# Performance work log

Hardware: AMD Instinct MI355X
Metric: run time of the kernel (lower is better)

The kernel has to match this reference:

```python
import jax, jax.numpy as jnp
import numpy as np

BETA = 0.25
N_EMBED = 8192
DIM = 256


def setup_inputs() -> dict:
    key = jax.random.key(0)
    k1, k2 = jax.random.split(key)
    z = jax.random.normal(k1, (16, DIM, 32, 32), dtype=jnp.float32)
    # nn.Embedding init: uniform(-1/n_embed, 1/n_embed)
    codebook = jax.random.uniform(
        k2, (N_EMBED, DIM), dtype=jnp.float32,
        minval=-1.0 / N_EMBED, maxval=1.0 / N_EMBED)
    return {"z": z, "codebook": codebook}


def reference(z, codebook):
    # b c h w -> b h w c
    zp = jnp.transpose(z, (0, 2, 3, 1))
    b, h, w, c = zp.shape
    zf = zp.reshape(-1, c)  # [N, dim]
    # squared L2 distances: ||z||^2 + ||e||^2 - 2 z.e
    d = (jnp.sum(zf * zf, axis=1, keepdims=True)
         + jnp.sum(codebook * codebook, axis=1)
         - 2.0 * jnp.einsum('nd,kd->nk', zf, codebook))  # [N, n_embed]
    idx = jnp.argmin(d, axis=1)  # [N]
    z_q = codebook[idx].reshape(b, h, w, c)
    loss = (BETA * jnp.mean((jax.lax.stop_gradient(z_q) - zp) ** 2)
            + jnp.mean((z_q - jax.lax.stop_gradient(zp)) ** 2))
    # straight-through estimator
    z_q = zp + jax.lax.stop_gradient(z_q - zp)
    z_q = jnp.transpose(z_q, (0, 3, 1, 2))  # b h w c -> b c h w
    return z_q, loss, idx
```

## Files before the change

kernel.cpp:

```cpp
#include <hip/hip_runtime.h>
#include <cfloat>


#define NROWS 16384
#define NCODE 8192
#define DIMC  256
#define HW    1024
#define ZQN   4194304

#define ZT_OFF   0
#define CBT_OFF  2097152
#define ZSQ_OFF  3145728
#define CAND_OFF 3162112
#define LOSS_OFF ZQN
#define IDX_OFF  (ZQN + 1)

#define NSLICE 8
#define PRUNE_T 4300u
#define ZSCALE 2097152.0f

typedef __attribute__((ext_vector_type(8))) short bf16x8;
typedef __attribute__((ext_vector_type(4))) float f32x4;
typedef __attribute__((ext_vector_type(4))) unsigned int uint4v;

__device__ __forceinline__ unsigned umax(unsigned a, unsigned b) { return a > b ? a : b; }
__device__ __forceinline__ unsigned umin(unsigned a, unsigned b) { return a < b ? a : b; }

__device__ __forceinline__ unsigned short f2bf(float f) {
    unsigned u = __float_as_uint(f);
    return (unsigned short)((u + 0x7fffu + ((u >> 16) & 1u)) >> 16);
}

#define GLD_LDS16(gptr, lptr) \
  __builtin_amdgcn_global_load_lds((const __attribute__((address_space(1))) unsigned int*)(const void*)(gptr), \
                                   (__attribute__((address_space(3))) unsigned int*)(lptr), 16, 0, 0)

__global__ void prep_kernel(const float* __restrict__ z, const float* __restrict__ cb,
                            float* __restrict__ out) {
    int bid = blockIdx.x;
    int tid = threadIdx.x;
    if (bid < 1024) {
        __shared__ unsigned short lds[64 * 65];
        unsigned short* zt = (unsigned short*)(out + ZT_OFF);
        int c0 = (bid & 3) * 64;
        int n0 = (bid >> 2) * 64;
        const float* zb = z + (size_t)(n0 >> 10) * (DIMC * HW) + (n0 & 1023);
        #pragma unroll
        for (int i = 0; i < 4; ++i) {
            int f = tid + i * 256;
            int cl = f >> 4, n4 = f & 15;
            float4 v = *(const float4*)(zb + (size_t)(c0 + cl) * HW + n4 * 4);
            lds[(n4 * 4 + 0) * 65 + cl] = f2bf(v.x * ZSCALE);
            lds[(n4 * 4 + 1) * 65 + cl] = f2bf(v.y * ZSCALE);
            lds[(n4 * 4 + 2) * 65 + cl] = f2bf(v.z * ZSCALE);
            lds[(n4 * 4 + 3) * 65 + cl] = f2bf(v.w * ZSCALE);
        }
        __syncthreads();
        #pragma unroll
        for (int i = 0; i < 2; ++i) {
            int f = tid + i * 256;
            int nl = f >> 3, oct = f & 7;
            const unsigned short* p = lds + nl * 65 + oct * 8;
            uint4v u;
            u.x = (unsigned)p[0] | ((unsigned)p[1] << 16);
            u.y = (unsigned)p[2] | ((unsigned)p[3] << 16);
            u.z = (unsigned)p[4] | ((unsigned)p[5] << 16);
            u.w = (unsigned)p[6] | ((unsigned)p[7] << 16);
            *(uint4v*)(zt + (size_t)(n0 + nl) * DIMC + c0 + oct * 8) = u;
        }
    } else if (bid < 2048) {
        unsigned short* cbt = (unsigned short*)(out + CBT_OFF);
        size_t t = (size_t)(bid - 1024) * 256 + tid;
        float4 a = *(const float4*)(cb + t * 8);
        float4 b = *(const float4*)(cb + t * 8 + 4);
        uint4v u;
        u.x = (unsigned)f2bf(a.x) | ((unsigned)f2bf(a.y) << 16);
        u.y = (unsigned)f2bf(a.z) | ((unsigned)f2bf(a.w) << 16);
        u.z = (unsigned)f2bf(b.x) | ((unsigned)f2bf(b.y) << 16);
        u.w = (unsigned)f2bf(b.z) | ((unsigned)f2bf(b.w) << 16);
        *(uint4v*)(cbt + t * 8) = u;
        if (bid == 1024 && tid == 0) out[LOSS_OFF] = 0.0f;
    } else {
        int n = (bid - 2048) * 256 + tid;
        const float* zp = z + (size_t)(n >> 10) * (DIMC * HW) + (n & 1023);
        double s = 0.0;
        for (int c = 0; c < DIMC; ++c) {
            double v = (double)zp[(size_t)c * HW];
            s += v * v;
        }
        out[ZSQ_OFF + n] = (float)s;
    }
}

__global__ __launch_bounds__(256, 2)
void argmin_kernel(float* __restrict__ out) {
    __shared__ __align__(16) unsigned short a_s[2 * 32 * 256];
    const unsigned short* zt  = (const unsigned short*)(out + ZT_OFF);
    const unsigned short* cbt = (const unsigned short*)(out + CBT_OFF);
    unsigned* cand = (unsigned*)(out + CAND_OFF);

    int tid = threadIdx.x;
    int lane = tid & 63;
    int wv = tid >> 6;
    int col = lane & 15, qk = lane >> 4;
    int n0 = blockIdx.x * 256;
    int slice = blockIdx.y;

    bf16x8 B[4][8];
    #pragma unroll
    for (int rf = 0; rf < 4; ++rf)
        #pragma unroll
        for (int t = 0; t < 8; ++t)
            B[rf][t] = *(const bf16x8*)(zt + (size_t)(n0 + wv * 64 + rf * 16 + col) * DIMC
                                           + t * 32 + qk * 8);

    int rl2 = lane >> 5;
    int jsl = lane & 31;
    const unsigned short* srcb[4];
    #pragma unroll
    for (int c = 0; c < 4; ++c) {
        int rloc = (wv * 4 + c) * 2 + rl2;
        int src16 = jsl ^ (rloc & 7) ^ ((rloc & 8) >> 1);
        srcb[c] = cbt + ((size_t)slice * 1024 + rloc) * DIMC + src16 * 8;
    }

    unsigned U1[4] = {0, 0, 0, 0}, U2[4] = {0, 0, 0, 0};

    const unsigned sb = (unsigned)((col & 7) ^ ((col & 8) >> 1));
    const unsigned short* aoff[8];
    #pragma unroll
    for (int t = 0; t < 8; ++t)
        aoff[t] = a_s + col * 256 + (((unsigned)(qk + 4 * t)) ^ sb) * 8;

    f32x4 acc[4][2];
    const f32x4 BIASV = (f32x4){131072.0f, 131072.0f, 131072.0f, 131072.0f};

    auto stage = [&](int ch, int dsto) {
        const size_t off = (size_t)ch * 32 * DIMC;
        unsigned short* dst = a_s + dsto;
        #pragma unroll
        for (int c = 0; c < 4; ++c)
            GLD_LDS16(srcb[c] + off, dst + (wv * 4 + c) * 512);
    };

    auto epi1 = [&](unsigned tb) {
        #pragma unroll
        for (int rf = 0; rf < 4; ++rf)
            #pragma unroll
            for (int r = 0; r < 4; ++r) {
                unsigned bits = __float_as_uint(acc[rf][1][r]);
                unsigned u = (bits & 0xFFFFFF00u) | (tb - (unsigned)(4 + r));
                unsigned lo = umin(u, U1[rf]);
                U1[rf] = umax(u, U1[rf]);
                U2[rf] = umax(lo, U2[rf]);
            }
    };

    auto compute = [&](int bufs , unsigned tb) {
        #pragma unroll
        for (int rf = 0; rf < 4; ++rf) acc[rf][0] = BIASV;
        #pragma unroll
        for (int t = 0; t < 8; ++t) {
            bf16x8 af = *(const bf16x8*)(aoff[t] + bufs);
            acc[0][0] = __builtin_amdgcn_mfma_f32_16x16x32_bf16(af, B[0][t], acc[0][0], 0, 0, 0);
            acc[1][0] = __builtin_amdgcn_mfma_f32_16x16x32_bf16(af, B[1][t], acc[1][0], 0, 0, 0);
            acc[2][0] = __builtin_amdgcn_mfma_f32_16x16x32_bf16(af, B[2][t], acc[2][0], 0, 0, 0);
            acc[3][0] = __builtin_amdgcn_mfma_f32_16x16x32_bf16(af, B[3][t], acc[3][0], 0, 0, 0);
        }
        #pragma unroll
        for (int rf = 0; rf < 4; ++rf) acc[rf][1] = BIASV;
        #pragma unroll
        for (int t = 0; t < 8; ++t) {
            bf16x8 af = *(const bf16x8*)(aoff[t] + bufs + 4096);
            acc[0][1] = __builtin_amdgcn_mfma_f32_16x16x32_bf16(af, B[0][t], acc[0][1], 0, 0, 0);
            acc[1][1] = __builtin_amdgcn_mfma_f32_16x16x32_bf16(af, B[1][t], acc[1][1], 0, 0, 0);
            acc[2][1] = __builtin_amdgcn_mfma_f32_16x16x32_bf16(af, B[2][t], acc[2][1], 0, 0, 0);
            acc[3][1] = __builtin_amdgcn_mfma_f32_16x16x32_bf16(af, B[3][t], acc[3][1], 0, 0, 0);
            {
                const int q0 = 2 * t, q1 = 2 * t + 1;
                const int rfA = q0 >> 2, rA = q0 & 3;
                const int rfB = q1 >> 2, rB = q1 & 3;
                unsigned bitsA = __float_as_uint(acc[rfA][0][rA]);
                unsigned uA = (bitsA & 0xFFFFFF00u) | (tb - (unsigned)rA);
                unsigned loA = umin(uA, U1[rfA]);
                U1[rfA] = umax(uA, U1[rfA]);
                U2[rfA] = umax(loA, U2[rfA]);
                unsigned bitsB = __float_as_uint(acc[rfB][0][rB]);
                unsigned uB = (bitsB & 0xFFFFFF00u) | (tb - (unsigned)rB);
                unsigned loB = umin(uB, U1[rfB]);
                U1[rfB] = umax(uB, U1[rfB]);
                U2[rfB] = umax(loB, U2[rfB]);
            }
        }
    };

    stage(0, 0);
    __syncthreads();
    stage(1, 8192);
    compute(0, 255u);

    for (int ch = 1; ch < 31; ch += 2) {
        unsigned tb1 = 255u - ((unsigned)ch << 3);
        __syncthreads();
        stage(ch + 1, 0);
        epi1(tb1 + 8u);
        compute(8192, tb1);
        __syncthreads();
        stage(ch + 2, 8192);
        epi1(tb1);
        compute(0, tb1 - 8u);
    }
    {
        __syncthreads();
        epi1(255u - (30u << 3));
        compute(8192, 255u - (31u << 3));
        epi1(255u - (31u << 3));
    }

    #pragma unroll
    for (int rf = 0; rf < 4; ++rf) {
        unsigned t1 = 255u - (U1[rf] & 255u);
        unsigned c1 = (t1 >> 3) * 32 + ((t1 >> 2) & 1) * 16 + qk * 4 + (t1 & 3);
        unsigned x1 = ((((U1[rf] & 0xFFFFFF00u) - 0x47000000u) >> 3) << 10) | (1023u - c1);
        unsigned t2 = 255u - (U2[rf] & 255u);
        unsigned c2 = (t2 >> 3) * 32 + ((t2 >> 2) & 1) * 16 + qk * 4 + (t2 & 3);
        unsigned x2 = ((((U2[rf] & 0xFFFFFF00u) - 0x47000000u) >> 3) << 10) | (1023u - c2);
        unsigned p1 = __shfl_xor(x1, 16);
        unsigned p2 = __shfl_xor(x2, 16);
        unsigned s1 = umax(x1, p1), tm = umin(x1, p1);
        unsigned ym = umax(x2, p2), s4 = umin(x2, p2);
        unsigned s2 = umax(tm, ym), s3 = umin(tm, ym);
        unsigned r1 = umax(s1, __shfl_xor(s4, 32));
        unsigned r2 = umax(s2, __shfl_xor(s3, 32));
        unsigned r3 = umax(s3, __shfl_xor(s2, 32));
        unsigned r4 = umax(s4, __shfl_xor(s1, 32));
        if (qk == 0) {
            int row = wv * 64 + rf * 16 + col;
            uint4v cw; cw.x = r1; cw.y = r2; cw.z = r3; cw.w = r4;
            *(uint4v*)(cand + ((size_t)slice * NROWS + n0 + row) * 4) = cw;
        }
    }
}

__global__ __launch_bounds__(256, 4)
void fixup_kernel(const float* __restrict__ z, const float* __restrict__ cb,
                  float* __restrict__ out) {
    __shared__ double zd[DIMC * 8];
    __shared__ float zsq_s[8];
    __shared__ unsigned qmx[8];
    __shared__ float dsc[32 * 8];
    __shared__ unsigned cds[32 * 8];
    int tid = threadIdx.x;
    int n0 = blockIdx.x * 8;
    const float* zb = z + (size_t)(n0 >> 10) * (DIMC * HW) + (n0 & 1023);
    int rr = tid & 7;
    #pragma unroll
    for (int i = 0; i < 8; ++i) {
        int c = (tid >> 3) + i * 32;
        zd[c * 8 + rr] = (double)zb[(size_t)c * HW + rr];
    }
    if (tid < 8) { zsq_s[tid] = out[ZSQ_OFF + n0 + tid]; qmx[tid] = 0; }
    int j = tid >> 3, r = tid & 7;
    unsigned w = ((const unsigned*)(out + CAND_OFF))
                 [(((size_t)(j >> 2)) * NROWS + n0 + r) * 4 + (j & 3)];
    unsigned qv = w >> 10;
    unsigned code = (unsigned)((j >> 2) * 1024) + 1023u - (w & 1023u);
    __syncthreads();
    atomicMax(&qmx[r], qv);
    __syncthreads();
    bool live = (qv + PRUNE_T >= qmx[r]);
    float d = FLT_MAX;
    if (live) {
        const float* e = cb + (size_t)code * DIMC;
        double a0 = 0.0, a1 = 0.0, a2 = 0.0, a3 = 0.0;
        for (int c = 0; c < DIMC; c += 16) {
            float4 e0 = *(const float4*)(e + c);
            float4 e1 = *(const float4*)(e + c + 4);
            float4 e2 = *(const float4*)(e + c + 8);
            float4 e3 = *(const float4*)(e + c + 12);
            a0 += zd[(c + 0) * 8 + r] * (double)e0.x + zd[(c + 1) * 8 + r] * (double)e0.y
                + zd[(c + 2) * 8 + r] * (double)e0.z + zd[(c + 3) * 8 + r] * (double)e0.w;
            a1 += zd[(c + 4) * 8 + r] * (double)e1.x + zd[(c + 5) * 8 + r] * (double)e1.y
                + zd[(c + 6) * 8 + r] * (double)e1.z + zd[(c + 7) * 8 + r] * (double)e1.w;
            a2 += zd[(c + 8) * 8 + r] * (double)e2.x + zd[(c + 9) * 8 + r] * (double)e2.y
                + zd[(c + 10) * 8 + r] * (double)e2.z + zd[(c + 11) * 8 + r] * (double)e2.w;
            a3 += zd[(c + 12) * 8 + r] * (double)e3.x + zd[(c + 13) * 8 + r] * (double)e3.y
                + zd[(c + 14) * 8 + r] * (double)e3.z + zd[(c + 15) * 8 + r] * (double)e3.w;
        }
        d = fmaf(-2.0f, (float)((a0 + a1) + (a2 + a3)), zsq_s[r]);
    }
    dsc[j * 8 + r] = d;
    cds[j * 8 + r] = code;
    __syncthreads();
    if (tid < 8) {
        float bd = FLT_MAX; unsigned bi = 0xffffffffu;
        for (int jj = 0; jj < 32; ++jj) {
            float dv = dsc[jj * 8 + tid];
            unsigned k = cds[jj * 8 + tid];
            if (dv < bd || (dv == bd && k < bi)) { bd = dv; bi = k; }
        }
        out[IDX_OFF + n0 + tid] = (float)bi;
    }
}

__global__ void zq_kernel(const float* __restrict__ z, const float* __restrict__ cb,
                          float* __restrict__ out) {
    __shared__ float lds[64 * 256];
    int tid = threadIdx.x;
    int n0 = blockIdx.x * 64;
    {
        int r = tid >> 2, q = tid & 3;
        int code = (int)out[IDX_OFF + n0 + r];
        const float* e = cb + (size_t)code * DIMC + q * 64;
        #pragma unroll
        for (int i = 0; i < 16; ++i) {
            float4 v = *(const float4*)(e + i * 4);
            int c4 = q * 16 + i;
            *(float4*)(lds + r * 256 + ((c4 ^ (r & 7)) * 4)) = v;
        }
    }
    __syncthreads();
    int hwl = tid & 63, g = tid >> 6;
    int b = n0 >> 10, hw0 = n0 & 1023;
    const size_t obase = (size_t)b * (DIMC * HW) + hw0 + hwl;
    float lsum = 0.f;
    #pragma unroll
    for (int i = 0; i < 16; ++i) {
        int c4 = g * 16 + i;
        float4 v = *(const float4*)(lds + hwl * 256 + ((c4 ^ (hwl & 7)) * 4));
        int c0 = c4 * 4;
        float z0 = z[obase + (size_t)(c0 + 0) * HW];
        float z1 = z[obase + (size_t)(c0 + 1) * HW];
        float z2 = z[obase + (size_t)(c0 + 2) * HW];
        float z3 = z[obase + (size_t)(c0 + 3) * HW];
        out[obase + (size_t)(c0 + 0) * HW] = v.x;
        out[obase + (size_t)(c0 + 1) * HW] = v.y;
        out[obase + (size_t)(c0 + 2) * HW] = v.z;
        out[obase + (size_t)(c0 + 3) * HW] = v.w;
        float d0 = v.x - z0, d1 = v.y - z1, d2 = v.z - z2, d3 = v.w - z3;
        lsum = fmaf(d0, d0, lsum); lsum = fmaf(d1, d1, lsum);
        lsum = fmaf(d2, d2, lsum); lsum = fmaf(d3, d3, lsum);
    }
    #pragma unroll
    for (int off = 32; off; off >>= 1) lsum += __shfl_down(lsum, off);
    __shared__ float red[4];
    if ((tid & 63) == 0) red[tid >> 6] = lsum;
    __syncthreads();
    if (tid == 0)
        atomicAdd(out + LOSS_OFF,
                  (red[0] + red[1] + red[2] + red[3]) * (1.25f / 4194304.0f));
}

extern "C" void kernel_launch(void* const* d_in, const int* in_sizes, int n_in,
                              void* d_out, int out_size, void* d_ws, size_t ws_size,
                              hipStream_t stream) {
    const float* z  = (const float*)d_in[0];
    const float* cb = (const float*)d_in[1];
    float* out = (float*)d_out;

    prep_kernel<<<2112, 256, 0, stream>>>(z, cb, out);
    argmin_kernel<<<dim3(64, NSLICE), 256, 0, stream>>>(out);
    fixup_kernel<<<NROWS / 8, 256, 0, stream>>>(z, cb, out);
    zq_kernel<<<256, 256, 0, stream>>>(z, cb, out);
}
```

Measured before the change: 184.8 us.

## Triple-buffer codebook chunks in LDS with vmcnt-based waits

The argmin kernel's LDS staging grows from two to three buffers, so codebook chunks are prefetched two chunks ahead instead of one. Each `__syncthreads` is replaced by an explicit `s_waitcnt vmcnt(4)` plus `s_barrier`. A wave then waits only for the oldest outstanding direct-to-LDS load rather than all of them, which should hide more global-load latency behind the MFMA work. In exchange LDS per block rises from 32KB to 48KB, which could limit occupancy. The hand-counted vmcnt also depends on each stage issuing exactly four loads.

Measured after the change: 184.5 us. No clear change (-0.1%).

```diff
diff --git a/kernel.cpp b/kernel.cpp
--- a/kernel.cpp
+++ b/kernel.cpp
@@ -94,7 +94,7 @@
 
 __global__ __launch_bounds__(256, 2)
 void argmin_kernel(float* __restrict__ out) {
-    __shared__ __align__(16) unsigned short a_s[2 * 32 * 256];
+    __shared__ __align__(16) unsigned short a_s[3 * 8192];
     const unsigned short* zt  = (const unsigned short*)(out + ZT_OFF);
     const unsigned short* cbt = (const unsigned short*)(out + CBT_OFF);
     unsigned* cand = (unsigned*)(out + CAND_OFF);
@@ -135,7 +135,7 @@
     f32x4 acc[4][2];
     const f32x4 BIASV = (f32x4){131072.0f, 131072.0f, 131072.0f, 131072.0f};
 
-    auto stage = [&](int ch, int dsto) {
+    auto stage = [&](int ch, int dsto ) {
         const size_t off = (size_t)ch * 32 * DIMC;
         unsigned short* dst = a_s + dsto;
         #pragma unroll
@@ -156,12 +156,12 @@
             }
     };
 
-    auto compute = [&](int bufs , unsigned tb) {
+    auto compute = [&](int bufb, unsigned tb) {
         #pragma unroll
         for (int rf = 0; rf < 4; ++rf) acc[rf][0] = BIASV;
         #pragma unroll
         for (int t = 0; t < 8; ++t) {
-            bf16x8 af = *(const bf16x8*)(aoff[t] + bufs);
+            bf16x8 af = *(const bf16x8*)((const char*)aoff[t] + bufb);
             acc[0][0] = __builtin_amdgcn_mfma_f32_16x16x32_bf16(af, B[0][t], acc[0][0], 0, 0, 0);
             acc[1][0] = __builtin_amdgcn_mfma_f32_16x16x32_bf16(af, B[1][t], acc[1][0], 0, 0, 0);
             acc[2][0] = __builtin_amdgcn_mfma_f32_16x16x32_bf16(af, B[2][t], acc[2][0], 0, 0, 0);
@@ -171,7 +171,7 @@
         for (int rf = 0; rf < 4; ++rf) acc[rf][1] = BIASV;
         #pragma unroll
         for (int t = 0; t < 8; ++t) {
-            bf16x8 af = *(const bf16x8*)(aoff[t] + bufs + 4096);
+            bf16x8 af = *(const bf16x8*)((const char*)aoff[t] + bufb + 8192);
             acc[0][1] = __builtin_amdgcn_mfma_f32_16x16x32_bf16(af, B[0][t], acc[0][1], 0, 0, 0);
             acc[1][1] = __builtin_amdgcn_mfma_f32_16x16x32_bf16(af, B[1][t], acc[1][1], 0, 0, 0);
             acc[2][1] = __builtin_amdgcn_mfma_f32_16x16x32_bf16(af, B[2][t], acc[2][1], 0, 0, 0);
@@ -194,28 +194,40 @@
         }
     };
 
+#define CHUNK_SYNC(N)                                          \
+    asm volatile("s_waitcnt vmcnt(" #N ")" ::: "memory");      \
+    __builtin_amdgcn_s_barrier();                              \
+    __builtin_amdgcn_sched_barrier(0);
+
     stage(0, 0);
-    __syncthreads();
     stage(1, 8192);
+
+    CHUNK_SYNC(4)
+    stage(2, 16384);
     compute(0, 255u);
 
-    for (int ch = 1; ch < 31; ch += 2) {
-        unsigned tb1 = 255u - ((unsigned)ch << 3);
-        __syncthreads();
-        stage(ch + 1, 0);
-        epi1(tb1 + 8u);
-        compute(8192, tb1);
-        __syncthreads();
-        stage(ch + 2, 8192);
-        epi1(tb1);
-        compute(0, tb1 - 8u);
-    }
-    {
-        __syncthreads();
-        epi1(255u - (30u << 3));
-        compute(8192, 255u - (31u << 3));
-        epi1(255u - (31u << 3));
-    }
+    #pragma unroll 1
+    for (int k = 0; k < 10; ++k) {
+        const int c1 = 3 * k + 1;
+        const unsigned tb = 255u - ((unsigned)c1 << 3);
+        CHUNK_SYNC(4)
+        stage(c1 + 2, 0);
+        epi1(tb + 8u);
+        compute(16384, tb);
+        CHUNK_SYNC(4)
+        stage(c1 + 3, 8192);
+        epi1(tb);
+        compute(32768, tb - 8u);
+        CHUNK_SYNC(4)
+        if (k < 9) stage(c1 + 4, 16384);
+        epi1(tb - 8u);
+        compute(0, tb - 16u);
+    }
+    CHUNK_SYNC(0)
+    epi1(255u - (30u << 3));
+    compute(16384, 255u - (31u << 3));
+    epi1(255u - (31u << 3));
+#undef CHUNK_SYNC
 
     #pragma unroll
     for (int rf = 0; rf < 4; ++rf) {
```
